# Kernel tuning notes

Measured on AMD Instinct MI355X. Metric: run time of the kernel, lower is better.

Reference implementation:

```python
import jax, jax.numpy as jnp
import numpy as np
import math

EMBED_DIM = 1024
NUM_HEADS = 16
HEAD_DIM = EMBED_DIM // NUM_HEADS


def setup_inputs() -> dict:
    key = jax.random.key(0)
    ks = jax.random.split(key, 5)
    x = jax.random.normal(ks[0], (4, 2048, EMBED_DIM), dtype=jnp.float32)
    # Linear params (torch nn.Linear: y = x @ W.T + b); init scale ~ 1/sqrt(fan_in)
    s = 1.0 / math.sqrt(EMBED_DIM)
    qkv_w = jax.random.uniform(ks[1], (3 * EMBED_DIM, EMBED_DIM), jnp.float32, -s, s)
    qkv_b = jax.random.uniform(ks[2], (3 * EMBED_DIM,), jnp.float32, -s, s)
    proj_w = jax.random.uniform(ks[3], (EMBED_DIM, EMBED_DIM), jnp.float32, -s, s)
    proj_b = jax.random.uniform(ks[4], (EMBED_DIM,), jnp.float32, -s, s)
    return {"x": x, "qkv_w": qkv_w, "qkv_b": qkv_b, "proj_w": proj_w, "proj_b": proj_b}


def reference(x, qkv_w, qkv_b, proj_w, proj_b):
    bsz, num_tokens, dim = x.shape
    qkv = x @ qkv_w.T + qkv_b  # [B, S, 3*D]
    qkv = qkv.reshape(bsz, num_tokens, 3, NUM_HEADS, HEAD_DIM)
    qkv = jnp.transpose(qkv, (2, 0, 3, 1, 4))  # [3, B, H, S, hd]
    q, k, v = qkv[0], qkv[1], qkv[2]
    scale = 1.0 / math.sqrt(HEAD_DIM)
    attn_scores = jnp.einsum('bhqd,bhkd->bhqk', q, k) * scale  # [B, H, S, S]
    attn = jax.nn.softmax(attn_scores, axis=-1)
    out = jnp.einsum('bhqk,bhkd->bhqd', attn, v)  # [B, H, S, hd]
    out = jnp.transpose(out, (0, 2, 1, 3)).reshape(bsz, num_tokens, dim)
    out = out @ proj_w.T + proj_b
    return out
```

## Files before the change

### kernel.cpp

```cpp
#include <hip/hip_runtime.h>
#include <stdint.h>

#define DEVICE static __device__ __forceinline__

typedef __bf16 bf16x8 __attribute__((ext_vector_type(8)));
typedef float f32x4 __attribute__((ext_vector_type(4)));

#define AS1 __attribute__((address_space(1)))
#define AS3 __attribute__((address_space(3)))

DEVICE void g2l16(const void* gptr, void* lptr) {
  __builtin_amdgcn_global_load_lds((AS1 uint32_t*)(uintptr_t)gptr,
                                   (AS3 uint32_t*)(uint32_t)(uintptr_t)lptr,
                                   16, 0, 0);
}

DEVICE float b2f(ushort h) {
  union { uint32_t u; float f; } v;
  v.u = ((uint32_t)h) << 16;
  return v.f;
}
DEVICE ushort f2b(float f) {
  union { float f; uint32_t u; } v;
  v.f = f;
  uint32_t u = v.u;
  return (ushort)((u + 0x7FFFu + ((u >> 16) & 1u)) >> 16);
}

#if defined(__has_builtin) && __has_builtin(__builtin_amdgcn_exp2f)
DEVICE float fast_exp2(float x) { return __builtin_amdgcn_exp2f(x); }
#else
extern "C" __device__ float __ocml_native_exp2_f32(float);
DEVICE float fast_exp2(float x) { return __ocml_native_exp2_f32(x); }
#endif

#define QSCALE 0.1803368801111244f

DEVICE int kperm(int x) {
  return (x & 0x23) | ((x & 0x18) >> 1) | ((x & 0x4) << 2);
}

__global__ void detect_dtype(const ushort* __restrict__ xu, int* __restrict__ flag) {
  __shared__ int bad;
  if (threadIdx.x == 0) bad = 0;
  __syncthreads();
  int mybad = 0;
#pragma unroll
  for (int j = 0; j < 8; ++j) {
    const int i = threadIdx.x * 8 + j;
    const ushort u = xu[2 * i];
    const int e = (u >> 7) & 0xFF;
    if (!(e == 0 || (e >= 96 && e <= 160))) mybad++;
  }
  atomicAdd(&bad, mybad);
  __syncthreads();
  if (threadIdx.x == 0) *flag = (bad > 512) ? 1 : 0;
}

__global__ void convert_all(const void* __restrict__ s0, const void* __restrict__ s1,
                            const void* __restrict__ s2, const void* __restrict__ s3,
                            const void* __restrict__ s4,
                            ushort* __restrict__ d0, ushort* __restrict__ d1,
                            ushort* __restrict__ d2, ushort* __restrict__ d3,
                            ushort* __restrict__ d4,
                            const int* __restrict__ flag) {
  const bool isf32 = (*flag != 0);
  for (int g = blockIdx.x * blockDim.x + threadIdx.x; g < 1573376;
       g += gridDim.x * blockDim.x) {
    const void* src; ushort* dst; int i;
    if (g < 1048576)      { src = s0; dst = d0; i = g; }
    else if (g < 1441792) { src = s1; dst = d1; i = g - 1048576; }
    else if (g < 1442176) { src = s2; dst = d2; i = g - 1441792; }
    else if (g < 1573248) { src = s3; dst = d3; i = g - 1442176; }
    else                  { src = s4; dst = d4; i = g - 1573248; }
    ushort pk[8];
    if (isf32) {
      const float4 a = ((const float4*)src)[2 * i];
      const float4 b = ((const float4*)src)[2 * i + 1];
      pk[0] = f2b(a.x); pk[1] = f2b(a.y); pk[2] = f2b(a.z); pk[3] = f2b(a.w);
      pk[4] = f2b(b.x); pk[5] = f2b(b.y); pk[6] = f2b(b.z); pk[7] = f2b(b.w);
      *(uint4*)&dst[8 * i] = *(const uint4*)pk;
    } else {
      *(uint4*)&dst[8 * i] = ((const uint4*)src)[i];
    }
  }
}

template <int MODE, int GN>
__global__ __launch_bounds__(512, 4)
void gemm256(const ushort* __restrict__ A, const ushort* __restrict__ W,
             const ushort* __restrict__ bias, ushort* __restrict__ O0,
             ushort* __restrict__ O1, ushort* __restrict__ O2,
             int M, int N, int K, const int* __restrict__ flag)
{
  __shared__ __align__(16) char smem[49152];

  const int tid = threadIdx.x;
  const int lane = tid & 63;
  const int wave = tid >> 6;
  const int quad = lane >> 4;
  const int lo = lane & 15;

  const int lin = blockIdx.y * gridDim.x + blockIdx.x;
  const int per = GN * gridDim.y;
  const int grp = lin / per;
  const int w   = lin % per;
  const int bxn = grp * GN + (w % GN);
  const int bym = w / GN;
  const int m0 = bym * 128;
  const int n0 = bxn * 256;

  const int wm = (wave >> 2) * 64;
  const int wn = (wave & 3) * 64;

  const int rA = tid >> 2;
  const int gA = (tid & 3) << 3;
  const size_t offA  = (size_t)(m0 + rA) * K + gA;
  const size_t offB0 = (size_t)(n0 + rA) * K + gA;
  const size_t offB1 = (size_t)(n0 + 128 + rA) * K + gA;
  const int dA = wave << 10;
  const int NT = K >> 5;

  f32x4 acc[4][4] = {};

  g2l16(A + offA,  smem + dA);
  g2l16(W + offB0, smem + 8192 + dA);
  g2l16(W + offB1, smem + 16384 + dA);
  asm volatile("s_waitcnt vmcnt(0)" ::: "memory");
  __builtin_amdgcn_s_barrier();

  for (int kt = 0; kt < NT; ++kt) {
    const char* buf = smem + (kt & 1) * 24576;
    const ushort* Al = (const ushort*)buf;
    const ushort* Bl = (const ushort*)(buf + 8192);
    const bool pf = (kt + 1 < NT);
    char* nbuf = smem + ((kt + 1) & 1) * 24576;
    const size_t nk = (size_t)(kt + 1) * 32;

    if (pf) {
      g2l16(A + offA  + nk, nbuf + dA);
      g2l16(W + offB0 + nk, nbuf + 8192 + dA);
    }
    bf16x8 bfr[4], af[2];
#pragma unroll
    for (int nt = 0; nt < 4; ++nt)
      bfr[nt] = *(const bf16x8*)&Bl[(wn + nt * 16 + lo) * 32 + quad * 8];
#pragma unroll
    for (int mt = 0; mt < 2; ++mt)
      af[mt] = *(const bf16x8*)&Al[(wm + mt * 16 + lo) * 32 + quad * 8];
    __builtin_amdgcn_s_setprio(1);
#pragma unroll
    for (int mt = 0; mt < 2; ++mt)
#pragma unroll
      for (int nt = 0; nt < 4; ++nt)
        acc[mt][nt] = __builtin_amdgcn_mfma_f32_16x16x32_bf16(
            af[mt], bfr[nt], acc[mt][nt], 0, 0, 0);
    __builtin_amdgcn_s_setprio(0);
    __builtin_amdgcn_s_barrier();

    if (pf)
      g2l16(W + offB1 + nk, nbuf + 16384 + dA);
    bf16x8 af2[2];
#pragma unroll
    for (int mt = 0; mt < 2; ++mt)
      af2[mt] = *(const bf16x8*)&Al[(wm + (mt + 2) * 16 + lo) * 32 + quad * 8];
    __builtin_amdgcn_s_setprio(1);
#pragma unroll
    for (int mt = 0; mt < 2; ++mt)
#pragma unroll
      for (int nt = 0; nt < 4; ++nt)
        acc[mt + 2][nt] = __builtin_amdgcn_mfma_f32_16x16x32_bf16(
            af2[mt], bfr[nt], acc[mt + 2][nt], 0, 0, 0);
    __builtin_amdgcn_s_setprio(0);

    if (kt < NT - 1) {
      asm volatile("s_waitcnt vmcnt(0)" ::: "memory");
      __builtin_amdgcn_s_barrier();
    }
  }

  if (MODE == 0) {
    const int which = n0 >> 10;
    if (which == 2) {
#pragma unroll
      for (int nt = 0; nt < 4; ++nt) {
        const int n = n0 + wn + nt * 16 + lo;
        const float bv = b2f(bias[n]);
        const int h = (n >> 6) & 15;
        const int d = n & 63;
#pragma unroll
        for (int mt = 0; mt < 4; ++mt) {
          const int m = m0 + wm + mt * 16 + quad * 4;
          const int b = m >> 11, s0 = m & 2047;
          ushort pk[4];
#pragma unroll
          for (int r = 0; r < 4; ++r) pk[r] = f2b(acc[mt][nt][r] + bv);
          *(uint2*)&O2[((size_t)(b * 16 + h) * 64 + d) * 2048 + s0] =
              *(const uint2*)pk;
        }
      }
    } else {
      const float qs = (which == 0) ? QSCALE : 1.0f;
      ushort* __restrict__ dst = (which == 0) ? O0 : O1;
      const int h = ((n0 + wn) >> 6) & 15;
      __syncthreads();
      ushort* scr = (ushort*)(smem + wave * 5632);
      float bv[4];
#pragma unroll
      for (int nt = 0; nt < 4; ++nt) bv[nt] = b2f(bias[n0 + wn + nt * 16 + lo]);
#pragma unroll
      for (int c2 = 0; c2 < 2; ++c2) {
#pragma unroll
        for (int mtl = 0; mtl < 2; ++mtl)
#pragma unroll
          for (int nt = 0; nt < 4; ++nt)
#pragma unroll
            for (int r = 0; r < 4; ++r)
              scr[(mtl * 16 + quad * 4 + r) * 88 + nt * 16 + lo] =
                  f2b((acc[c2 * 2 + mtl][nt][r] + bv[nt]) * qs);
        asm volatile("s_waitcnt lgkmcnt(0)" ::: "memory");
#pragma unroll
        for (int i = 0; i < 4; ++i) {
          const int id = lane + 64 * i;
          const int rowl = id >> 3, nch = id & 7;
          const uint4 val = *(const uint4*)&scr[rowl * 88 + nch * 8];
          const int m = m0 + wm + c2 * 32 + rowl;
          const int b = m >> 11;
          int s = m & 2047;
          if (which == 1) s = (s & ~63) | kperm(s & 63);
          *(uint4*)&dst[((size_t)(b * 16 + h) * 2048 + s) * 64 + nch * 8] = val;
        }
      }
    }
  } else {
    const bool f32out = (*flag != 0);
    float* Of = (float*)O0;
#pragma unroll
    for (int nt = 0; nt < 4; ++nt) {
      const int n = n0 + wn + nt * 16 + lo;
      const float bv = b2f(bias[n]);
#pragma unroll
      for (int mt = 0; mt < 4; ++mt)
#pragma unroll
        for (int r = 0; r < 4; ++r) {
          const int m = m0 + wm + mt * 16 + quad * 4 + r;
          const float val = acc[mt][nt][r] + bv;
          if (f32out) Of[(size_t)m * N + n] = val;
          else        O0[(size_t)m * N + n] = f2b(val);
        }
    }
  }
}

__global__ __launch_bounds__(256, 4)
void attn_fwd(const ushort* __restrict__ qp, const ushort* __restrict__ kp,
              const ushort* __restrict__ vp, ushort* __restrict__ o)
{
  __shared__ ushort Qs[128 * 64];
  __shared__ ushort Ks[64 * 64];
  __shared__ ushort Vt[64 * 64];

  const int tid = threadIdx.x;
  const int lane = tid & 63;
  const int wave = tid >> 6;
  const int quad = lane >> 4;
  const int lo = lane & 15;
  const int sw = (lo & 7) << 3;

  const int lin = blockIdx.y * gridDim.x + blockIdx.x;
  const int bh = (lin & 7) * 8 + ((lin >> 3) & 7);
  const int q0 = (lin >> 6) * 128;

  const ushort* Qg = qp + (size_t)bh * 2048 * 64;
  const ushort* Kg = kp + (size_t)bh * 2048 * 64;
  const ushort* Vg = vp + (size_t)bh * 64 * 2048;

#pragma unroll
  for (int i = 0; i < 4; ++i) {
    const int c = tid + 256 * i;
    const int row = c >> 3;
    const int kc = ((c ^ row) & 7) << 3;
    g2l16(Qg + (size_t)(q0 + row) * 64 + kc,
          (char*)Qs + ((wave << 6) + (i << 8)) * 16);
  }
  __syncthreads();

  bf16x8 qf[2][2];
#pragma unroll
  for (int mt = 0; mt < 2; ++mt)
#pragma unroll
    for (int ks = 0; ks < 2; ++ks)
      qf[mt][ks] = *(const bf16x8*)&Qs[(wave * 32 + mt * 16 + lo) * 64 +
                                       ((ks * 32 + quad * 8) ^ sw)];

  bf16x8 ones;
#pragma unroll
  for (int j = 0; j < 8; ++j) ones[j] = (__bf16)1.0f;

  f32x4 oacc[2][4] = {};
  f32x4 sumacc[2] = {};

  for (int j0 = 0; j0 < 2048; j0 += 64) {
    __syncthreads();
#pragma unroll
    for (int i = 0; i < 2; ++i) {
      const int c = tid + 256 * i;
      const int row = c >> 3;
      const int kc = ((c ^ row) & 7) << 3;
      g2l16(Kg + (size_t)(j0 + row) * 64 + kc,
            (char*)Ks + ((wave << 6) + (i << 8)) * 16);
      g2l16(Vg + (size_t)row * 2048 + j0 + kc,
            (char*)Vt + ((wave << 6) + (i << 8)) * 16);
    }
    __syncthreads();

    f32x4 sacc[2][4] = {};
#pragma unroll
    for (int ks = 0; ks < 2; ++ks) {
#pragma unroll
      for (int nt = 0; nt < 4; ++nt) {
        const bf16x8 kf =
            *(const bf16x8*)&Ks[(nt * 16 + lo) * 64 + ((ks * 32 + quad * 8) ^ sw)];
#pragma unroll
        for (int mt = 0; mt < 2; ++mt)
          sacc[mt][nt] = __builtin_amdgcn_mfma_f32_16x16x32_bf16(
              kf, qf[mt][ks], sacc[mt][nt], 0, 0, 0);
      }
    }

    bf16x8 pfr[2][2];
#pragma unroll
    for (int mt = 0; mt < 2; ++mt) {
      float p[4][4];
#pragma unroll
      for (int nt = 0; nt < 4; ++nt)
#pragma unroll
        for (int r = 0; r < 4; ++r)
          p[nt][r] = fast_exp2(sacc[mt][nt][r]);
#pragma unroll
      for (int b = 0; b < 2; ++b)
#pragma unroll
        for (int h = 0; h < 2; ++h)
#pragma unroll
          for (int r = 0; r < 4; ++r)
            pfr[mt][b][4 * h + r] = (__bf16)p[2 * b + h][r];
    }

#pragma unroll
    for (int b = 0; b < 2; ++b) {
#pragma unroll
      for (int mt = 0; mt < 2; ++mt)
        sumacc[mt] = __builtin_amdgcn_mfma_f32_16x16x32_bf16(
            pfr[mt][b], ones, sumacc[mt], 0, 0, 0);
#pragma unroll
      for (int dt = 0; dt < 4; ++dt) {
        const bf16x8 vf =
            *(const bf16x8*)&Vt[(dt * 16 + lo) * 64 + ((b * 32 + quad * 8) ^ sw)];
#pragma unroll
        for (int mt = 0; mt < 2; ++mt)
          oacc[mt][dt] = __builtin_amdgcn_mfma_f32_16x16x32_bf16(
              pfr[mt][b], vf, oacc[mt][dt], 0, 0, 0);
      }
    }
  }

  const int b_ = bh >> 4;
  const int h = bh & 15;
#pragma unroll
  for (int mt = 0; mt < 2; ++mt) {
#pragma unroll
    for (int r = 0; r < 4; ++r) {
      const float inv = 1.0f / sumacc[mt][r];
      const int srow = q0 + wave * 32 + mt * 16 + quad * 4 + r;
#pragma unroll
      for (int dt = 0; dt < 4; ++dt) {
        o[(((size_t)(b_ * 2048 + srow)) << 10) + h * 64 + dt * 16 + lo] =
            f2b(oacc[mt][dt][r] * inv);
      }
    }
  }
}

extern "C" void kernel_launch(void* const* d_in, const int* in_sizes, int n_in,
                              void* d_out, int out_size, void* d_ws, size_t ws_size,
                              hipStream_t stream) {
  const size_t N_X  = (size_t)4 * 2048 * 1024;
  const size_t N_WQ = (size_t)3072 * 1024;
  const size_t N_BQ = 3072;
  const size_t N_WP = (size_t)1024 * 1024;
  const size_t N_BP = 1024;
  const size_t HSD  = (size_t)64 * 2048 * 64;

  ushort* xb = (ushort*)d_ws;
  ushort* wq = xb + N_X;
  ushort* bq = wq + N_WQ;
  ushort* wp = bq + N_BQ;
  ushort* bp = wp + N_WP;
  ushort* qb = bp + N_BP;
  ushort* kb = qb + HSD;
  ushort* vb = kb + HSD;
  ushort* ab = vb + HSD;
  int* flag  = (int*)(ab + HSD);

  detect_dtype<<<1, 256, 0, stream>>>((const ushort*)d_in[0], flag);
  convert_all<<<2048, 256, 0, stream>>>(d_in[0], d_in[1], d_in[2], d_in[3], d_in[4],
                                        xb, wq, bq, wp, bp, flag);

  gemm256<0, 4><<<dim3(12, 64), dim3(512), 0, stream>>>(
      xb, wq, bq, qb, kb, vb, 8192, 3072, 1024, flag);
  attn_fwd<<<dim3(16, 64), dim3(256), 0, stream>>>(qb, kb, vb, ab);
  gemm256<1, 4><<<dim3(4, 64), dim3(512), 0, stream>>>(
      ab, wp, bp, (ushort*)d_out, nullptr, nullptr, 8192, 1024, 1024, flag);
}
```

Baseline: 263.2 us.

## Double-buffer K/V tiles in attention and swizzle GEMM LDS layout

The attention kernel now keeps two LDS buffers for K and V and prefetches the next 64-key tile while computing on the current one. This replaces the two barriers per iteration with a single wait-and-barrier at the end of each iteration. Separately, the GEMM XOR-swizzles the 16-byte k-chunk position in LDS on both the global-to-LDS write side and the fragment read side, to reduce bank conflicts. Double buffering doubles K/V LDS use (from 16 KB to 32 KB, plus 16 KB for Q), which may lower attention occupancy.

```diff
diff --git a/kernel.cpp b/kernel.cpp
--- a/kernel.cpp
+++ b/kernel.cpp
@@ -100,6 +100,7 @@
   const int wave = tid >> 6;
   const int quad = lane >> 4;
   const int lo = lane & 15;
+  const int kch = (quad ^ ((lo >> 1) & 3)) << 3;
 
   const int lin = blockIdx.y * gridDim.x + blockIdx.x;
   const int per = GN * gridDim.y;
@@ -114,7 +115,7 @@
   const int wn = (wave & 3) * 64;
 
   const int rA = tid >> 2;
-  const int gA = (tid & 3) << 3;
+  const int gA = (((tid & 3) ^ ((tid >> 3) & 3)) << 3);
   const size_t offA  = (size_t)(m0 + rA) * K + gA;
   const size_t offB0 = (size_t)(n0 + rA) * K + gA;
   const size_t offB1 = (size_t)(n0 + 128 + rA) * K + gA;
@@ -144,10 +145,10 @@
     bf16x8 bfr[4], af[2];
 #pragma unroll
     for (int nt = 0; nt < 4; ++nt)
-      bfr[nt] = *(const bf16x8*)&Bl[(wn + nt * 16 + lo) * 32 + quad * 8];
+      bfr[nt] = *(const bf16x8*)&Bl[(wn + nt * 16 + lo) * 32 + kch];
 #pragma unroll
     for (int mt = 0; mt < 2; ++mt)
-      af[mt] = *(const bf16x8*)&Al[(wm + mt * 16 + lo) * 32 + quad * 8];
+      af[mt] = *(const bf16x8*)&Al[(wm + mt * 16 + lo) * 32 + kch];
     __builtin_amdgcn_s_setprio(1);
 #pragma unroll
     for (int mt = 0; mt < 2; ++mt)
@@ -163,7 +164,7 @@
     bf16x8 af2[2];
 #pragma unroll
     for (int mt = 0; mt < 2; ++mt)
-      af2[mt] = *(const bf16x8*)&Al[(wm + (mt + 2) * 16 + lo) * 32 + quad * 8];
+      af2[mt] = *(const bf16x8*)&Al[(wm + (mt + 2) * 16 + lo) * 32 + kch];
     __builtin_amdgcn_s_setprio(1);
 #pragma unroll
     for (int mt = 0; mt < 2; ++mt)
@@ -257,8 +258,8 @@
               const ushort* __restrict__ vp, ushort* __restrict__ o)
 {
   __shared__ ushort Qs[128 * 64];
-  __shared__ ushort Ks[64 * 64];
-  __shared__ ushort Vt[64 * 64];
+  __shared__ ushort Ks2[2][64 * 64];
+  __shared__ ushort Vt2[2][64 * 64];
 
   const int tid = threadIdx.x;
   const int lane = tid & 63;
@@ -283,7 +284,18 @@
     g2l16(Qg + (size_t)(q0 + row) * 64 + kc,
           (char*)Qs + ((wave << 6) + (i << 8)) * 16);
   }
-  __syncthreads();
+#pragma unroll
+  for (int i = 0; i < 2; ++i) {
+    const int c = tid + 256 * i;
+    const int row = c >> 3;
+    const int kc = ((c ^ row) & 7) << 3;
+    g2l16(Kg + (size_t)row * 64 + kc,
+          (char*)Ks2[0] + ((wave << 6) + (i << 8)) * 16);
+    g2l16(Vg + (size_t)row * 2048 + kc,
+          (char*)Vt2[0] + ((wave << 6) + (i << 8)) * 16);
+  }
+  asm volatile("s_waitcnt vmcnt(0)" ::: "memory");
+  __builtin_amdgcn_s_barrier();
 
   bf16x8 qf[2][2];
 #pragma unroll
@@ -300,19 +312,24 @@
   f32x4 oacc[2][4] = {};
   f32x4 sumacc[2] = {};
 
-  for (int j0 = 0; j0 < 2048; j0 += 64) {
-    __syncthreads();
-#pragma unroll
-    for (int i = 0; i < 2; ++i) {
-      const int c = tid + 256 * i;
-      const int row = c >> 3;
-      const int kc = ((c ^ row) & 7) << 3;
-      g2l16(Kg + (size_t)(j0 + row) * 64 + kc,
-            (char*)Ks + ((wave << 6) + (i << 8)) * 16);
-      g2l16(Vg + (size_t)row * 2048 + j0 + kc,
-            (char*)Vt + ((wave << 6) + (i << 8)) * 16);
-    }
-    __syncthreads();
+  for (int t = 0; t < 32; ++t) {
+    const int cur = t & 1;
+    const ushort* Kc = Ks2[cur];
+    const ushort* Vc = Vt2[cur];
+
+    if (t < 31) {
+      const int j1 = (t + 1) * 64;
+#pragma unroll
+      for (int i = 0; i < 2; ++i) {
+        const int c = tid + 256 * i;
+        const int row = c >> 3;
+        const int kc = ((c ^ row) & 7) << 3;
+        g2l16(Kg + (size_t)(j1 + row) * 64 + kc,
+              (char*)Ks2[cur ^ 1] + ((wave << 6) + (i << 8)) * 16);
+        g2l16(Vg + (size_t)row * 2048 + j1 + kc,
+              (char*)Vt2[cur ^ 1] + ((wave << 6) + (i << 8)) * 16);
+      }
+    }
 
     f32x4 sacc[2][4] = {};
 #pragma unroll
@@ -320,7 +337,7 @@
 #pragma unroll
       for (int nt = 0; nt < 4; ++nt) {
         const bf16x8 kf =
-            *(const bf16x8*)&Ks[(nt * 16 + lo) * 64 + ((ks * 32 + quad * 8) ^ sw)];
+            *(const bf16x8*)&Kc[(nt * 16 + lo) * 64 + ((ks * 32 + quad * 8) ^ sw)];
 #pragma unroll
         for (int mt = 0; mt < 2; ++mt)
           sacc[mt][nt] = __builtin_amdgcn_mfma_f32_16x16x32_bf16(
@@ -355,13 +372,16 @@
 #pragma unroll
       for (int dt = 0; dt < 4; ++dt) {
         const bf16x8 vf =
-            *(const bf16x8*)&Vt[(dt * 16 + lo) * 64 + ((b * 32 + quad * 8) ^ sw)];
+            *(const bf16x8*)&Vc[(dt * 16 + lo) * 64 + ((b * 32 + quad * 8) ^ sw)];
 #pragma unroll
         for (int mt = 0; mt < 2; ++mt)
           oacc[mt][dt] = __builtin_amdgcn_mfma_f32_16x16x32_bf16(
               pfr[mt][b], vf, oacc[mt][dt], 0, 0, 0);
       }
     }
+
+    asm volatile("s_waitcnt vmcnt(0)" ::: "memory");
+    __builtin_amdgcn_s_barrier();
   }
 
   const int b_ = bh >> 4;
```

Result: slower. 279.6 us (+6.2%).
